# Optimization experiments

Hardware: AMD Instinct MI355X
Metric: run time of the kernel (lower is better)

Reference implementation:

```python
import jax, jax.numpy as jnp
import numpy as np

N_FRAMES = 4
HEADS = 8
SEQ = 576
DIM = 640


def setup_inputs() -> dict:
    key = jax.random.key(0)
    ks = jax.random.split(key, 6)
    x = jax.random.normal(ks[0], (3 * N_FRAMES, SEQ, DIM), dtype=jnp.float32)
    s = 1.0 / np.sqrt(DIM)
    Wq = jax.random.normal(ks[1], (DIM, DIM), dtype=jnp.float32) * s
    Wk = jax.random.normal(ks[2], (DIM, DIM), dtype=jnp.float32) * s
    Wv = jax.random.normal(ks[3], (DIM, DIM), dtype=jnp.float32) * s
    Wo = jax.random.normal(ks[4], (DIM, DIM), dtype=jnp.float32) * s
    bo = jnp.zeros((DIM,), dtype=jnp.float32)
    return {"x": x, "Wq": Wq, "Wk": Wk, "Wv": Wv, "Wo": Wo, "bo": bo}


def reference(x, Wq, Wk, Wv, Wo, bo):
    # x: [3F, S, D] -- stacked [source | uncond | cond] frame batches
    B, S, D = x.shape
    n = B // 3                       # n_frames
    h = HEADS
    hd = D // h
    scale = 1.0 / jnp.sqrt(jnp.asarray(hd, x.dtype))

    # torch nn.Linear: y = x @ W.T
    q = jnp.einsum('bsd,ed->bse', x, Wq)
    k = jnp.einsum('bsd,ed->bse', x, Wk)
    v = jnp.einsum('bsd,ed->bse', x, Wv)

    def heads_fd(t):  # [F,S,D] -> [F,h,S,hd]
        return t.reshape(t.shape[0], S, h, hd).transpose(0, 2, 1, 3)

    def heads_flat(t):  # [F,S,D] -> [h, F*S, hd]  (shared across all query frames)
        return t.reshape(t.shape[0] * S, h, hd).transpose(1, 0, 2)

    # ---- source: per-frame self-attention ----
    qs, ks_, vs = heads_fd(q[:n]), heads_fd(k[:n]), heads_fd(v[:n])
    sim_s = jnp.einsum('fhqd,fhkd->fhqk', qs, ks_) * scale
    out_s = jnp.einsum('fhqk,fhkd->fhqd', jax.nn.softmax(sim_s, axis=-1), vs)

    # ---- uncond / cond: each frame attends to concatenated KV of all frames ----
    def cross_frame(q_chunk, k_chunk, v_chunk):
        qf = heads_fd(q_chunk)          # [F,h,S,hd]
        kf = heads_flat(k_chunk)        # [h,F*S,hd]
        vf = heads_flat(v_chunk)        # [h,F*S,hd]
        sim = jnp.einsum('fhqd,hkd->fhqk', qf, kf) * scale   # [F,h,S,F*S]
        return jnp.einsum('fhqk,hkd->fhqd', jax.nn.softmax(sim, axis=-1), vf)

    out_u = cross_frame(q[n:2 * n], k[n:2 * n], v[n:2 * n])
    out_c = cross_frame(q[2 * n:], k[2 * n:], v[2 * n:])

    out = jnp.concatenate([out_s, out_u, out_c], axis=0)      # [3F,h,S,hd]
    out = out.transpose(0, 2, 1, 3).reshape(B, S, D)          # merge heads
    return jnp.einsum('bsd,ed->bse', out, Wo) + bo
```

## Files before the change

kernel.cpp:

```cpp
#include <hip/hip_runtime.h>
#include <hip/hip_bf16.h>

#define SEQ    576
#define DIM    640
#define HEADS  8
#define HD     80
#define NF     4
#define NB     12
#define M_TOT  (NB * SEQ)
#define SCALE  0.11180339887498949f
#define LOG2E  1.4426950408889634f

typedef __attribute__((ext_vector_type(8))) short          bf16x8;
typedef __attribute__((ext_vector_type(4))) float          f32x4;
typedef __attribute__((ext_vector_type(8))) unsigned short u16x8;
typedef __attribute__((ext_vector_type(4))) unsigned short u16x4;

__device__ __forceinline__ unsigned short f2bf(float x) {
    unsigned u = __float_as_uint(x);
    u += 0x7fffu + ((u >> 16) & 1u);
    return (unsigned short)(u >> 16);
}
__device__ __forceinline__ float bf2f(unsigned short h) {
    return __uint_as_float((unsigned)h << 16);
}
__device__ __forceinline__ f32x4 mfma16(bf16x8 a, bf16x8 b, f32x4 c) {
    return __builtin_amdgcn_mfma_f32_16x16x32_bf16(a, b, c, 0, 0, 0);
}
__device__ __forceinline__ float fexp2(float x) {
    return __builtin_amdgcn_exp2f(x);
}
__device__ __forceinline__ void dma16(const void* g, void* s) {
    __builtin_amdgcn_global_load_lds(
        (const __attribute__((address_space(1))) void*)g,
        (__attribute__((address_space(3))) void*)s, 16, 0, 0);
}

__global__ __launch_bounds__(256) void split_kernel(
    const float* __restrict__ X,  const float* __restrict__ Wq,
    const float* __restrict__ Wk, const float* __restrict__ Wv,
    const float* __restrict__ Wo,
    unsigned short* __restrict__ Xh,  unsigned short* __restrict__ Wqh,
    unsigned short* __restrict__ Wkh, unsigned short* __restrict__ Wvh,
    unsigned short* __restrict__ Woh)
{
    const int z = blockIdx.y;
    const float* src; unsigned short* dh; int n; float s = 1.0f;
    switch (z) {
        case 0:  src = X;  dh = Xh;  n = M_TOT * DIM; break;
        case 1:  src = Wq; dh = Wqh; n = DIM * DIM; s = SCALE * LOG2E; break;
        case 2:  src = Wk; dh = Wkh; n = DIM * DIM; break;
        case 3:  src = Wv; dh = Wvh; n = DIM * DIM; break;
        default: src = Wo; dh = Woh; n = DIM * DIM; break;
    }
    const int base = blockIdx.x * 4096 + threadIdx.x * 16;
    if (base >= n) return;
#pragma unroll
    for (int half = 0; half < 2; ++half) {
        const int b = base + half * 8;
        float4 a4 = *(const float4*)(src + b);
        float4 b4 = *(const float4*)(src + b + 4);
        float vv[8] = {a4.x, a4.y, a4.z, a4.w, b4.x, b4.y, b4.z, b4.w};
        union { unsigned short u[8]; u16x8 v; } ph;
#pragma unroll
        for (int j = 0; j < 8; ++j) ph.u[j] = f2bf(vv[j] * s);
        *(u16x8*)(dh + b) = ph.v;
    }
}

__global__ __launch_bounds__(256) void qkv_mfma_kernel(
    const unsigned short* __restrict__ Xh,
    const unsigned short* __restrict__ Wqh, const unsigned short* __restrict__ Wkh,
    const unsigned short* __restrict__ Wvh,
    unsigned short* __restrict__ Qh,
    unsigned short* __restrict__ Kb, unsigned short* __restrict__ VtG)
{
    __shared__ unsigned short smem[2][10240];

    const int flat = blockIdx.x + 27 * (blockIdx.y + 10 * blockIdx.z);
    const int xcd  = flat & 7;
    const int slot = flat >> 3;
    const int l    = (xcd < 2 ? xcd * 102 : 204 + (xcd - 2) * 101) + slot;
    const int m_idx = l / 30;
    const int rem   = l - m_idx * 30;
    const int z     = rem / 10;
    const int n_idx = rem - z * 10;

    const unsigned short* WH = (z == 0) ? Wqh : ((z == 1) ? Wkh : Wvh);
    const int m0 = m_idx * 256;
    const int n0 = n_idx * 64;

    const int t    = threadIdx.x;
    const int w    = t >> 6;
    const int lane = t & 63;
    const int quad = lane >> 4;
    const int ln   = lane & 15;

    f32x4 acc[4][4];
#pragma unroll
    for (int mi = 0; mi < 4; ++mi)
#pragma unroll
        for (int nt = 0; nt < 4; ++nt)
#pragma unroll
            for (int e = 0; e < 4; ++e) acc[mi][nt][e] = 0.f;

    const int lr = lane >> 2;
    const int lc = (lane & 3) * 8;

    auto stage = [&](int buf, int k0) {
        unsigned short* As = smem[buf];
        unsigned short* Bs = smem[buf] + 8192;
        const unsigned short* gp = Xh + (size_t)(m0 + w * 64 + lr) * DIM + k0 + lc;
#pragma unroll
        for (int i = 0; i < 4; ++i)
            dma16(gp + (size_t)i * 16 * DIM, &As[(w * 64 + i * 16) * 32]);
        const size_t gb = (size_t)(n0 + w * 16 + lr) * DIM + k0 + lc;
        dma16(WH + gb, &Bs[w * 16 * 32]);
    };

    stage(0, 0);
    __syncthreads();

    for (int k0 = 0; k0 < DIM; k0 += 32) {
        const int kb = (k0 >> 5) & 1;
        if (k0 + 32 < DIM) stage(kb ^ 1, k0 + 32);

        const unsigned short* As = smem[kb];
        const unsigned short* Bs = smem[kb] + 8192;
        bf16x8 af[4];
#pragma unroll
        for (int mi = 0; mi < 4; ++mi)
            af[mi] = *(const bf16x8*)&As[(w * 64 + mi * 16 + ln) * 32 + quad * 8];
#pragma unroll
        for (int nt = 0; nt < 4; ++nt) {
            bf16x8 bh = *(const bf16x8*)&Bs[(nt * 16 + ln) * 32 + quad * 8];
#pragma unroll
            for (int mi = 0; mi < 4; ++mi)
                acc[mi][nt] = mfma16(af[mi], bh, acc[mi][nt]);
        }
        __syncthreads();
    }

    if (z == 0) {
#pragma unroll
        for (int mi = 0; mi < 4; ++mi)
#pragma unroll
            for (int r = 0; r < 4; ++r) {
                const size_t row = m0 + w * 64 + mi * 16 + quad * 4 + r;
#pragma unroll
                for (int nt = 0; nt < 4; ++nt)
                    Qh[row * DIM + n0 + nt * 16 + ln] = f2bf(acc[mi][nt][r]);
            }
    } else if (z == 1) {
#pragma unroll
        for (int mi = 0; mi < 4; ++mi)
#pragma unroll
            for (int r = 0; r < 4; ++r) {
                const size_t row = m0 + w * 64 + mi * 16 + quad * 4 + r;
#pragma unroll
                for (int nt = 0; nt < 4; ++nt)
                    Kb[row * DIM + n0 + nt * 16 + ln] = f2bf(acc[mi][nt][r]);
            }
    } else {
        unsigned short* Vts = smem[0];
#pragma unroll 1
        for (int half = 0; half < 2; ++half) {
            __syncthreads();
            if ((w >> 1) == half) {
                const int wl = w & 1;
#pragma unroll
                for (int mi = 0; mi < 4; ++mi)
#pragma unroll
                    for (int nt = 0; nt < 4; ++nt)
#pragma unroll
                        for (int r = 0; r < 4; ++r)
                            Vts[(nt * 16 + ln) * 136 + wl * 64 + mi * 16 + quad * 4 + r] =
                                f2bf(acc[mi][nt][r]);
            }
            __syncthreads();
            const int nn = t & 63;
            const int c0 = (t >> 6) * 32;
#pragma unroll
            for (int i = 0; i < 4; ++i)
                *(u16x8*)(VtG + (size_t)(n0 + nn) * M_TOT + m0 + half * 128 + c0 + i * 8) =
                    *(const u16x8*)&Vts[nn * 136 + c0 + i * 8];
        }
    }
}

__global__ __launch_bounds__(256, 2) void attn_mfma_kernel(
    const unsigned short* __restrict__ Qh,
    const unsigned short* __restrict__ Kb, const unsigned short* __restrict__ Vt,
    unsigned short* __restrict__ Oh,
    unsigned short* __restrict__ Pn, float2* __restrict__ ml)
{
    const int flat = blockIdx.x + 3 * (blockIdx.y + 8 * blockIdx.z);
    const int h    = flat & 7;
    const int slot = flat >> 3;
    const int z    = slot / 3;
    const int qt   = slot - z * 3;

    int f, kbase, nkt, idx = -1;
    if (z < 16) {
        idx = z;
        const int fi = z >> 1;
        f = 4 + fi;
        kbase = ((fi < 4 ? 4 : 8) + (z & 1) * 2) * SEQ;
        nkt = 18;
    } else {
        f = z - 16;
        kbase = f * SEQ;
        nkt = 9;
    }

    const int t    = threadIdx.x;
    const int w    = t >> 6;
    const int lane = t & 63;
    const int quad = lane >> 4;
    const int ln   = lane & 15;

    __shared__ unsigned short KhS[2][12 * 64 * 8];
    __shared__ unsigned short VtS[2][80 * 64];
    __shared__ unsigned short Pb[4 * 48 * 72];

    bf16x8 qf[3][3];
#pragma unroll
    for (int mi = 0; mi < 3; ++mi) {
        const int qrow = f * SEQ + qt * 192 + w * 48 + mi * 16 + ln;
        const unsigned short* qp = Qh + (size_t)qrow * DIM + h * HD;
#pragma unroll
        for (int kc = 0; kc < 3; ++kc) {
            const int dbase = kc * 32 + quad * 8;
            if (dbase < HD) {
                qf[mi][kc] = *(const bf16x8*)(qp + dbase);
            } else {
                union { unsigned short u[8]; bf16x8 v; } zz;
#pragma unroll
                for (int j = 0; j < 8; ++j) zz.u[j] = 0;
                qf[mi][kc] = zz.v;
            }
        }
    }

    auto stage_k = [&](int buf, int kvt) {
        const unsigned short* kg = Kb + (size_t)(kbase + kvt * 64) * DIM + h * HD;
#pragma unroll
        for (int rnd = 0; rnd < 3; ++rnd) {
            const int g = rnd * 4 + w;
            dma16(kg + (size_t)lane * DIM + g * 8, &KhS[buf][g * 512]);
        }
    };
    u16x8 vreg[3];
    auto load_v = [&](int kvt) {
#pragma unroll
        for (int i = 0; i < 3; ++i) {
            const int u = t + i * 256;
            if (u < 640) {
                const int d = u >> 3, c8 = u & 7;
                vreg[i] = *(const u16x8*)(Vt + (size_t)(h * HD + d) * M_TOT +
                                          kbase + kvt * 64 + c8 * 8);
            }
        }
    };
    auto write_v = [&](int buf) {
#pragma unroll
        for (int i = 0; i < 3; ++i) {
            const int u = t + i * 256;
            if (u < 640) {
                const int d = u >> 3, c8 = u & 7;
                const int c8s = (c8 + 3 * d) & 7;
                *(u16x8*)&VtS[buf][d * 64 + c8s * 8] = vreg[i];
            }
        }
    };

    float m_[3], l_[3];
#pragma unroll
    for (int mi = 0; mi < 3; ++mi) { m_[mi] = -INFINITY; l_[mi] = 0.f; }

    f32x4 oacc[3][5];
#pragma unroll
    for (int mi = 0; mi < 3; ++mi)
#pragma unroll
        for (int nt = 0; nt < 5; ++nt)
#pragma unroll
            for (int e = 0; e < 4; ++e) oacc[mi][nt][e] = 0.f;

    unsigned short* PbW = &Pb[w * 48 * 72];

    stage_k(0, 0);
    load_v(0);
    write_v(0);
    __syncthreads();

    for (int kt = 0; kt < nkt; ++kt) {
        const int cur = kt & 1;
        const bool pf = (kt + 1 < nkt);

        if (pf) {
            load_v(kt + 1);
            stage_k(cur ^ 1, kt + 1);
        }

        f32x4 sacc[3][4];
#pragma unroll
        for (int mi = 0; mi < 3; ++mi)
#pragma unroll
            for (int nt = 0; nt < 4; ++nt)
#pragma unroll
                for (int e = 0; e < 4; ++e) sacc[mi][nt][e] = 0.f;
#pragma unroll
        for (int nt = 0; nt < 4; ++nt)
#pragma unroll
            for (int kc = 0; kc < 3; ++kc) {
                bf16x8 kf = *(const bf16x8*)&KhS[cur][((kc * 4 + quad) * 64 +
                                                      nt * 16 + ln) * 8];
#pragma unroll
                for (int mi = 0; mi < 3; ++mi)
                    sacc[mi][nt] = mfma16(kf, qf[mi][kc], sacc[mi][nt]);
            }

        float mxl[3];
#pragma unroll
        for (int mi = 0; mi < 3; ++mi) {
            float t0[4];
#pragma unroll
            for (int nt = 0; nt < 4; ++nt)
                t0[nt] = fmaxf(fmaxf(sacc[mi][nt][0], sacc[mi][nt][1]),
                               fmaxf(sacc[mi][nt][2], sacc[mi][nt][3]));
            mxl[mi] = fmaxf(fmaxf(t0[0], t0[1]), fmaxf(t0[2], t0[3]));
        }
        const bool need = (mxl[0] > m_[0] + 8.0f) || (mxl[1] > m_[1] + 8.0f) ||
                          (mxl[2] > m_[2] + 8.0f);
        if (__any(need)) {
#pragma unroll
            for (int mi = 0; mi < 3; ++mi) {
                float mx = fmaxf(mxl[mi], __shfl_xor(mxl[mi], 16));
                mx = fmaxf(mx, __shfl_xor(mx, 32));
                const float mnew = fmaxf(m_[mi], mx);
                const float aq = fexp2(m_[mi] - mnew);
                m_[mi] = mnew;
                l_[mi] *= aq;
#pragma unroll
                for (int r = 0; r < 4; ++r) {
                    const float ar = __shfl(aq, quad * 4 + r, 64);
#pragma unroll
                    for (int nt = 0; nt < 5; ++nt) oacc[mi][nt][r] *= ar;
                }
            }
        }
#pragma unroll
        for (int mi = 0; mi < 3; ++mi) {
            float s = 0.f;
#pragma unroll
            for (int nt = 0; nt < 4; ++nt) {
                const float p0 = fexp2(sacc[mi][nt][0] - m_[mi]);
                const float p1 = fexp2(sacc[mi][nt][1] - m_[mi]);
                const float p2 = fexp2(sacc[mi][nt][2] - m_[mi]);
                const float p3 = fexp2(sacc[mi][nt][3] - m_[mi]);
                s += (p0 + p1) + (p2 + p3);
                union { unsigned u32[2]; u16x4 v; } pk;
                pk.u32[0] = __builtin_amdgcn_perm(__float_as_uint(p1),
                                                  __float_as_uint(p0), 0x07060302u);
                pk.u32[1] = __builtin_amdgcn_perm(__float_as_uint(p3),
                                                  __float_as_uint(p2), 0x07060302u);
                *(u16x4*)&PbW[(mi * 16 + ln) * 72 + nt * 16 + quad * 4] = pk.v;
            }
            l_[mi] += s;
        }

        __threadfence_block();

#pragma unroll
        for (int kc = 0; kc < 2; ++kc) {
            bf16x8 pf_[3];
#pragma unroll
            for (int mi = 0; mi < 3; ++mi)
                pf_[mi] = *(const bf16x8*)&PbW[(mi * 16 + ln) * 72 + kc * 32 + quad * 8];
#pragma unroll
            for (int nt = 0; nt < 5; ++nt) {
                const int vrow = nt * 16 + ln;
                const int c8r  = ((kc * 4 + quad) + 3 * vrow) & 7;
                bf16x8 vf = *(const bf16x8*)&VtS[cur][vrow * 64 + c8r * 8];
#pragma unroll
                for (int mi = 0; mi < 3; ++mi)
                    oacc[mi][nt] = mfma16(pf_[mi], vf, oacc[mi][nt]);
            }
        }

        if (pf) write_v(cur ^ 1);
        __syncthreads();
    }

#pragma unroll
    for (int mi = 0; mi < 3; ++mi) {
        l_[mi] += __shfl_xor(l_[mi], 16);
        l_[mi] += __shfl_xor(l_[mi], 32);
    }
#pragma unroll
    for (int mi = 0; mi < 3; ++mi)
#pragma unroll
        for (int r = 0; r < 4; ++r) {
            const float lr_ = __shfl(l_[mi], quad * 4 + r, 64);
            const float inv = 1.f / lr_;
            const int rr = qt * 192 + w * 48 + mi * 16 + quad * 4 + r;
            if (idx < 0) {
                const size_t orow = (size_t)f * SEQ + rr;
#pragma unroll
                for (int nt = 0; nt < 5; ++nt)
                    Oh[orow * DIM + h * HD + nt * 16 + ln] = f2bf(oacc[mi][nt][r] * inv);
            } else {
#pragma unroll
                for (int nt = 0; nt < 5; ++nt)
                    Pn[((size_t)idx * SEQ + rr) * DIM + h * HD + nt * 16 + ln] =
                        f2bf(oacc[mi][nt][r] * inv);
            }
        }
    if (idx >= 0 && lane < 16) {
#pragma unroll
        for (int mi = 0; mi < 3; ++mi) {
            const int rr = qt * 192 + w * 48 + mi * 16 + lane;
            ml[((size_t)idx * 8 + h) * SEQ + rr] = make_float2(m_[mi], l_[mi]);
        }
    }
}

__global__ __launch_bounds__(320) void merge_kernel(
    const unsigned short* __restrict__ Pn, const float2* __restrict__ ml,
    unsigned short* __restrict__ Oh)
{
    const int row = blockIdx.x;
    const int fi  = blockIdx.y;
    const int t   = threadIdx.x;
    const int i0  = fi * 2, i1 = i0 + 1;
#pragma unroll
    for (int rep = 0; rep < 2; ++rep) {
        const int col = t + rep * 320;
        const int h = col / 80;
        const float2 a = ml[((size_t)i0 * 8 + h) * SEQ + row];
        const float2 b = ml[((size_t)i1 * 8 + h) * SEQ + row];
        const float M  = fmaxf(a.x, b.x);
        const float w0 = fexp2(a.x - M) * a.y;
        const float w1 = fexp2(b.x - M) * b.y;
        const float inv = 1.f / (w0 + w1);
        const float p0 = bf2f(Pn[((size_t)i0 * SEQ + row) * DIM + col]);
        const float p1 = bf2f(Pn[((size_t)i1 * SEQ + row) * DIM + col]);
        Oh[((size_t)(4 + fi) * SEQ + row) * DIM + col] = f2bf((w0 * p0 + w1 * p1) * inv);
    }
}

__global__ __launch_bounds__(256) void oproj_mfma_kernel(
    const unsigned short* __restrict__ Oh,
    const unsigned short* __restrict__ Woh,
    const float* __restrict__ bo, float* __restrict__ out)
{
    __shared__ unsigned short smem[2][10240];

    const int flat = blockIdx.x + 27 * blockIdx.y;
    const int xcd  = flat & 7;
    const int slot = flat >> 3;
    const int l    = (xcd < 6 ? xcd * 34 : 204 + (xcd - 6) * 33) + slot;
    const int m_idx = l / 10;
    const int n_idx = l - m_idx * 10;
    const int m0 = m_idx * 256;
    const int n0 = n_idx * 64;

    const int t    = threadIdx.x;
    const int w    = t >> 6;
    const int lane = t & 63;
    const int quad = lane >> 4;
    const int ln   = lane & 15;

    f32x4 acc[4][4];
#pragma unroll
    for (int mi = 0; mi < 4; ++mi)
#pragma unroll
        for (int nt = 0; nt < 4; ++nt)
#pragma unroll
            for (int e = 0; e < 4; ++e) acc[mi][nt][e] = 0.f;

    const int lr = lane >> 2;
    const int lc = (lane & 3) * 8;

    auto stage = [&](int buf, int k0) {
        unsigned short* As = smem[buf];
        unsigned short* Bs = smem[buf] + 8192;
        const unsigned short* gp = Oh + (size_t)(m0 + w * 64 + lr) * DIM + k0 + lc;
#pragma unroll
        for (int i = 0; i < 4; ++i)
            dma16(gp + (size_t)i * 16 * DIM, &As[(w * 64 + i * 16) * 32]);
        const size_t gb = (size_t)(n0 + w * 16 + lr) * DIM + k0 + lc;
        dma16(Woh + gb, &Bs[w * 16 * 32]);
    };

    stage(0, 0);
    __syncthreads();

    for (int k0 = 0; k0 < DIM; k0 += 32) {
        const int kb = (k0 >> 5) & 1;
        if (k0 + 32 < DIM) stage(kb ^ 1, k0 + 32);

        const unsigned short* As = smem[kb];
        const unsigned short* Bs = smem[kb] + 8192;
        bf16x8 af[4];
#pragma unroll
        for (int mi = 0; mi < 4; ++mi)
            af[mi] = *(const bf16x8*)&As[(w * 64 + mi * 16 + ln) * 32 + quad * 8];
#pragma unroll
        for (int nt = 0; nt < 4; ++nt) {
            bf16x8 bh = *(const bf16x8*)&Bs[(nt * 16 + ln) * 32 + quad * 8];
#pragma unroll
            for (int mi = 0; mi < 4; ++mi)
                acc[mi][nt] = mfma16(af[mi], bh, acc[mi][nt]);
        }
        __syncthreads();
    }

#pragma unroll
    for (int mi = 0; mi < 4; ++mi)
#pragma unroll
        for (int r = 0; r < 4; ++r) {
            const size_t row = m0 + w * 64 + mi * 16 + quad * 4 + r;
#pragma unroll
            for (int nt = 0; nt < 4; ++nt) {
                const int col = n0 + nt * 16 + ln;
                out[row * DIM + col] = acc[mi][nt][r] + bo[col];
            }
        }
}

extern "C" void kernel_launch(void* const* d_in, const int* in_sizes, int n_in,
                              void* d_out, int out_size, void* d_ws, size_t ws_size,
                              hipStream_t stream)
{
    const float* x  = (const float*)d_in[0];
    const float* Wq = (const float*)d_in[1];
    const float* Wk = (const float*)d_in[2];
    const float* Wv = (const float*)d_in[3];
    const float* Wo = (const float*)d_in[4];
    const float* bo = (const float*)d_in[5];
    float* out = (float*)d_out;

    const size_t NX = (size_t)M_TOT * DIM;
    const size_t NW = (size_t)DIM * DIM;
    unsigned short* p = (unsigned short*)d_ws;
    unsigned short* Wqh = p;  p += NW;
    unsigned short* Wkh = p;  p += NW;
    unsigned short* Wvh = p;  p += NW;
    unsigned short* Woh = p;  p += NW;
    unsigned short* Xh  = p;  p += NX;
    unsigned short* Qhb = p;  p += NX;
    unsigned short* Kbb = p;  p += NX;
    unsigned short* Vtb = p;  p += NX;
    unsigned short* Ohb = Xh;

    unsigned short* Pn = (unsigned short*)d_out;
    float2* ml = (float2*)((char*)d_out + (size_t)16 * SEQ * DIM * 2);

    dim3 g0((unsigned)((NX + 4095) / 4096), 5);
    split_kernel<<<g0, 256, 0, stream>>>(x, Wq, Wk, Wv, Wo,
        Xh, Wqh, Wkh, Wvh, Woh);

    dim3 g1(M_TOT / 256, DIM / 64, 3);
    qkv_mfma_kernel<<<g1, 256, 0, stream>>>(Xh, Wqh, Wkh, Wvh, Qhb, Kbb, Vtb);

    dim3 g2(3, HEADS, 20);
    attn_mfma_kernel<<<g2, 256, 0, stream>>>(Qhb, Kbb, Vtb, Ohb, Pn, ml);

    dim3 g3(SEQ, 8);
    merge_kernel<<<g3, 320, 0, stream>>>(Pn, ml, Ohb);

    dim3 g4(M_TOT / 256, DIM / 64);
    oproj_mfma_kernel<<<g4, 256, 0, stream>>>(Ohb, Woh, bo, out);
}
```

Before: 191.1 us.

## Keep softmax probabilities in registers via permuted K rows and transposed PV MFMA

Permutes the K rows loaded into LDS and swaps MFMA operand order so the S accumulator layout matches the B-operand layout needed for the P·V product. Probabilities can then be packed to bf16 directly in registers, which removes the per-warp LDS P buffer, its stores, the block fence and the reloads. Rescaling no longer needs per-row shuffles, and output stores become 4-wide vector writes. The risk is a mistake in the lane permutation, which would silently produce wrong attention results.

```diff
diff --git a/kernel.cpp b/kernel.cpp
--- a/kernel.cpp
+++ b/kernel.cpp
@@ -29,6 +29,9 @@
 }
 __device__ __forceinline__ float fexp2(float x) {
     return __builtin_amdgcn_exp2f(x);
+}
+__device__ __forceinline__ float max3f(float a, float b, float c) {
+    return fmaxf(fmaxf(a, b), c);
 }
 __device__ __forceinline__ void dma16(const void* g, void* s) {
     __builtin_amdgcn_global_load_lds(
@@ -221,7 +224,9 @@
 
     __shared__ unsigned short KhS[2][12 * 64 * 8];
     __shared__ unsigned short VtS[2][80 * 64];
-    __shared__ unsigned short Pb[4 * 48 * 72];
+
+    const int klane = (lane & 3) | (((lane >> 4) & 1) << 2) |
+                      (((lane >> 2) & 3) << 3) | (lane & 32);
 
     bf16x8 qf[3][3];
 #pragma unroll
@@ -247,7 +252,7 @@
 #pragma unroll
         for (int rnd = 0; rnd < 3; ++rnd) {
             const int g = rnd * 4 + w;
-            dma16(kg + (size_t)lane * DIM + g * 8, &KhS[buf][g * 512]);
+            dma16(kg + (size_t)klane * DIM + g * 8, &KhS[buf][g * 512]);
         }
     };
     u16x8 vreg[3];
@@ -286,8 +291,6 @@
 #pragma unroll
             for (int e = 0; e < 4; ++e) oacc[mi][nt][e] = 0.f;
 
-    unsigned short* PbW = &Pb[w * 48 * 72];
-
     stage_k(0, 0);
     load_v(0);
     write_v(0);
@@ -302,33 +305,32 @@
             stage_k(cur ^ 1, kt + 1);
         }
 
+        const f32x4 fz = {0.f, 0.f, 0.f, 0.f};
         f32x4 sacc[3][4];
 #pragma unroll
-        for (int mi = 0; mi < 3; ++mi)
-#pragma unroll
-            for (int nt = 0; nt < 4; ++nt)
-#pragma unroll
-                for (int e = 0; e < 4; ++e) sacc[mi][nt][e] = 0.f;
-#pragma unroll
-        for (int nt = 0; nt < 4; ++nt)
+        for (int nt = 0; nt < 4; ++nt) {
+            const int ks = ln + 16 * (nt >> 1) + 32 * (nt & 1);
 #pragma unroll
             for (int kc = 0; kc < 3; ++kc) {
-                bf16x8 kf = *(const bf16x8*)&KhS[cur][((kc * 4 + quad) * 64 +
-                                                      nt * 16 + ln) * 8];
+                bf16x8 kf = *(const bf16x8*)&KhS[cur][((kc * 4 + quad) * 64 + ks) * 8];
 #pragma unroll
                 for (int mi = 0; mi < 3; ++mi)
-                    sacc[mi][nt] = mfma16(kf, qf[mi][kc], sacc[mi][nt]);
-            }
+                    sacc[mi][nt] = (kc == 0)
+                        ? mfma16(kf, qf[mi][0], fz)
+                        : mfma16(kf, qf[mi][kc], sacc[mi][nt]);
+            }
+        }
 
         float mxl[3];
 #pragma unroll
         for (int mi = 0; mi < 3; ++mi) {
-            float t0[4];
-#pragma unroll
-            for (int nt = 0; nt < 4; ++nt)
-                t0[nt] = fmaxf(fmaxf(sacc[mi][nt][0], sacc[mi][nt][1]),
-                               fmaxf(sacc[mi][nt][2], sacc[mi][nt][3]));
-            mxl[mi] = fmaxf(fmaxf(t0[0], t0[1]), fmaxf(t0[2], t0[3]));
+            const f32x4* S = sacc[mi];
+            const float a = max3f(S[0][0], S[0][1], S[0][2]);
+            const float b = max3f(S[0][3], S[1][0], S[1][1]);
+            const float c = max3f(S[1][2], S[1][3], S[2][0]);
+            const float d = max3f(S[2][1], S[2][2], S[2][3]);
+            const float e = max3f(S[3][0], S[3][1], S[3][2]);
+            mxl[mi] = fmaxf(max3f(a, b, c), max3f(d, e, S[3][3]));
         }
         const bool need = (mxl[0] > m_[0] + 8.0f) || (mxl[1] > m_[1] + 8.0f) ||
                           (mxl[2] > m_[2] + 8.0f);
@@ -342,41 +344,48 @@
                 m_[mi] = mnew;
                 l_[mi] *= aq;
 #pragma unroll
-                for (int r = 0; r < 4; ++r) {
-                    const float ar = __shfl(aq, quad * 4 + r, 64);
-#pragma unroll
-                    for (int nt = 0; nt < 5; ++nt) oacc[mi][nt][r] *= ar;
-                }
-            }
-        }
+                for (int nt = 0; nt < 5; ++nt)
+#pragma unroll
+                    for (int e = 0; e < 4; ++e) oacc[mi][nt][e] *= aq;
+            }
+        }
+        bf16x8 pfv[3][2];
 #pragma unroll
         for (int mi = 0; mi < 3; ++mi) {
             float s = 0.f;
+            float p[4][4];
 #pragma unroll
             for (int nt = 0; nt < 4; ++nt) {
-                const float p0 = fexp2(sacc[mi][nt][0] - m_[mi]);
-                const float p1 = fexp2(sacc[mi][nt][1] - m_[mi]);
-                const float p2 = fexp2(sacc[mi][nt][2] - m_[mi]);
-                const float p3 = fexp2(sacc[mi][nt][3] - m_[mi]);
-                s += (p0 + p1) + (p2 + p3);
-                union { unsigned u32[2]; u16x4 v; } pk;
-                pk.u32[0] = __builtin_amdgcn_perm(__float_as_uint(p1),
-                                                  __float_as_uint(p0), 0x07060302u);
-                pk.u32[1] = __builtin_amdgcn_perm(__float_as_uint(p3),
-                                                  __float_as_uint(p2), 0x07060302u);
-                *(u16x4*)&PbW[(mi * 16 + ln) * 72 + nt * 16 + quad * 4] = pk.v;
-            }
+#pragma unroll
+                for (int r = 0; r < 4; ++r) {
+                    p[nt][r] = fexp2(sacc[mi][nt][r] - m_[mi]);
+                    s += p[nt][r];
+                }
+            }
+            union { unsigned w[4]; bf16x8 v; } u0, u1;
+            u0.w[0] = __builtin_amdgcn_perm(__float_as_uint(p[0][1]),
+                                            __float_as_uint(p[0][0]), 0x07060302u);
+            u0.w[1] = __builtin_amdgcn_perm(__float_as_uint(p[0][3]),
+                                            __float_as_uint(p[0][2]), 0x07060302u);
+            u0.w[2] = __builtin_amdgcn_perm(__float_as_uint(p[2][1]),
+                                            __float_as_uint(p[2][0]), 0x07060302u);
+            u0.w[3] = __builtin_amdgcn_perm(__float_as_uint(p[2][3]),
+                                            __float_as_uint(p[2][2]), 0x07060302u);
+            u1.w[0] = __builtin_amdgcn_perm(__float_as_uint(p[1][1]),
+                                            __float_as_uint(p[1][0]), 0x07060302u);
+            u1.w[1] = __builtin_amdgcn_perm(__float_as_uint(p[1][3]),
+                                            __float_as_uint(p[1][2]), 0x07060302u);
+            u1.w[2] = __builtin_amdgcn_perm(__float_as_uint(p[3][1]),
+                                            __float_as_uint(p[3][0]), 0x07060302u);
+            u1.w[3] = __builtin_amdgcn_perm(__float_as_uint(p[3][3]),
+                                            __float_as_uint(p[3][2]), 0x07060302u);
+            pfv[mi][0] = u0.v;
+            pfv[mi][1] = u1.v;
             l_[mi] += s;
         }
 
-        __threadfence_block();
-
-#pragma unroll
-        for (int kc = 0; kc < 2; ++kc) {
-            bf16x8 pf_[3];
-#pragma unroll
-            for (int mi = 0; mi < 3; ++mi)
-                pf_[mi] = *(const bf16x8*)&PbW[(mi * 16 + ln) * 72 + kc * 32 + quad * 8];
+#pragma unroll
+        for (int kc = 0; kc < 2; ++kc)
 #pragma unroll
             for (int nt = 0; nt < 5; ++nt) {
                 const int vrow = nt * 16 + ln;
@@ -384,9 +393,8 @@
                 bf16x8 vf = *(const bf16x8*)&VtS[cur][vrow * 64 + c8r * 8];
 #pragma unroll
                 for (int mi = 0; mi < 3; ++mi)
-                    oacc[mi][nt] = mfma16(pf_[mi], vf, oacc[mi][nt]);
-            }
-        }
+                    oacc[mi][nt] = mfma16(vf, pfv[mi][kc], oacc[mi][nt]);
+            }
 
         if (pf) write_v(cur ^ 1);
         __syncthreads();
@@ -398,24 +406,21 @@
         l_[mi] += __shfl_xor(l_[mi], 32);
     }
 #pragma unroll
-    for (int mi = 0; mi < 3; ++mi)
-#pragma unroll
-        for (int r = 0; r < 4; ++r) {
-            const float lr_ = __shfl(l_[mi], quad * 4 + r, 64);
-            const float inv = 1.f / lr_;
-            const int rr = qt * 192 + w * 48 + mi * 16 + quad * 4 + r;
-            if (idx < 0) {
-                const size_t orow = (size_t)f * SEQ + rr;
-#pragma unroll
-                for (int nt = 0; nt < 5; ++nt)
-                    Oh[orow * DIM + h * HD + nt * 16 + ln] = f2bf(oacc[mi][nt][r] * inv);
-            } else {
-#pragma unroll
-                for (int nt = 0; nt < 5; ++nt)
-                    Pn[((size_t)idx * SEQ + rr) * DIM + h * HD + nt * 16 + ln] =
-                        f2bf(oacc[mi][nt][r] * inv);
-            }
-        }
+    for (int mi = 0; mi < 3; ++mi) {
+        const float inv = 1.f / l_[mi];
+        const int rr = qt * 192 + w * 48 + mi * 16 + ln;
+#pragma unroll
+        for (int nt = 0; nt < 5; ++nt) {
+            union { unsigned short u[4]; u16x4 v; } o4;
+#pragma unroll
+            for (int r = 0; r < 4; ++r) o4.u[r] = f2bf(oacc[mi][nt][r] * inv);
+            const int dcol = h * HD + nt * 16 + quad * 4;
+            if (idx < 0)
+                *(u16x4*)&Oh[((size_t)f * SEQ + rr) * DIM + dcol] = o4.v;
+            else
+                *(u16x4*)&Pn[((size_t)idx * SEQ + rr) * DIM + dcol] = o4.v;
+        }
+    }
     if (idx >= 0 && lane < 16) {
 #pragma unroll
         for (int mi = 0; mi < 3; ++mi) {
```

Result: faster. 187.2 us (-2.1%).
